# Kernel tuning notes

Measured on AMD Instinct MI355X. Metric: run time of the kernel, lower is better.

The kernel has to match this reference:

```python
import jax, jax.numpy as jnp
import numpy as np

D_MODEL = 1024
N_HEADS = 16
D_HEAD = D_MODEL // N_HEADS
WINDOW = 64
SCALE = 1.0 / np.sqrt(D_HEAD)


def setup_inputs() -> dict:
    key = jax.random.key(0)
    k1, k2, k3 = jax.random.split(key, 3)
    B, N = 1, 4096
    x = jax.random.normal(k1, (B, N, D_MODEL), dtype=jnp.float32)
    # xavier-uniform-ish init for weights (scaled normal is fine for a numeric reference)
    w_qkv = jax.random.normal(k2, (3 * D_MODEL, D_MODEL), dtype=jnp.float32) * (1.0 / np.sqrt(D_MODEL))
    b_qkv = jnp.zeros((3 * D_MODEL,), dtype=jnp.float32)
    w_out = jax.random.normal(k3, (D_MODEL, D_MODEL), dtype=jnp.float32) * (1.0 / np.sqrt(D_MODEL))
    b_out = jnp.zeros((D_MODEL,), dtype=jnp.float32)
    return {"x": x, "w_qkv": w_qkv, "b_qkv": b_qkv, "w_out": w_out, "b_out": b_out}


def reference(x, w_qkv, b_qkv, w_out, b_out):
    B, N, D = x.shape
    # QKV projection (torch Linear: x @ W^T + b)
    qkv = x @ w_qkv.T + b_qkv                      # [B, N, 3D]
    qkv = qkv.reshape(B, N, 3, N_HEADS, D_HEAD)
    qkv = jnp.transpose(qkv, (2, 0, 3, 1, 4))       # [3, B, H, N, dh]
    q, k, v = qkv[0], qkv[1], qkv[2]
    # dense scores, masked to causal sliding window (faithful to original)
    scores = jnp.einsum('bhqd,bhkd->bhqk', q, k) * SCALE  # [B, H, N, N]
    qpos = jnp.arange(N)[:, None]
    kpos = jnp.arange(N)[None, :]
    diff = qpos - kpos
    mask = (diff >= 0) & (diff < WINDOW)            # [N, N]
    scores = jnp.where(mask[None, None, :, :], scores, -jnp.inf)
    attn = jax.nn.softmax(scores, axis=-1)          # every query has >=1 valid key (self)
    out = jnp.einsum('bhqk,bhkd->bhqd', attn, v)    # [B, H, N, dh]
    out = jnp.transpose(out, (0, 2, 1, 3)).reshape(B, N, D)
    out = out @ w_out.T + b_out
    return out
```

## Files before the change

kernel.cpp:

```cpp
#include <hip/hip_runtime.h>
#include <hip/hip_bf16.h>
#include <stdint.h>
#include <stddef.h>

#define NSEQ  4096
#define DM    1024
#define NHEAD 16
#define DHEAD 64
#define WIN   64

using short8 = __attribute__((ext_vector_type(8))) short;
using f32x4  = __attribute__((ext_vector_type(4))) float;

#define GLOBAL_AS __attribute__((address_space(1)))
#define LDS_AS    __attribute__((address_space(3)))

__device__ __forceinline__ unsigned short f2bf(float f) {
  union { float f; unsigned int u; } v; v.f = f;
  unsigned int r = v.u + 0x7FFFu + ((v.u >> 16) & 1u);
  return (unsigned short)(r >> 16);
}

__device__ __forceinline__ void gload_lds16(void* lds, const void* g) {
  __builtin_amdgcn_global_load_lds((const GLOBAL_AS unsigned int*)g,
                                   (LDS_AS unsigned int*)lds, 16, 0, 0);
}

#define NX4 1048576
#define NW4 786432
__global__ void cvt_all(const float* __restrict__ x,
                        const float* __restrict__ wqkv,
                        const float* __restrict__ wout,
                        unsigned short* __restrict__ dst) {
  int i = blockIdx.x * blockDim.x + threadIdx.x;
  float4 f;
  if (i < NX4)            f = ((const float4*)x)[i];
  else if (i < NX4 + NW4) f = ((const float4*)wqkv)[i - NX4];
  else                    f = ((const float4*)wout)[i - (NX4 + NW4)];
  ushort4 o;
  o.x = f2bf(f.x); o.y = f2bf(f.y); o.z = f2bf(f.z); o.w = f2bf(f.w);
  ((ushort4*)dst)[i] = o;
}

__global__ __launch_bounds__(512, 1)
void gemm_qkv(const unsigned short* __restrict__ A,
              const unsigned short* __restrict__ B,
              const float* __restrict__ bias,
              unsigned short* __restrict__ qo,
              unsigned short* __restrict__ ko,
              unsigned short* __restrict__ vo) {
  __shared__ short lds[57344];

  const int bm = blockIdx.x >> 4;
  const int bn = blockIdx.x & 15;
  const int m0 = bm << 8, n0 = bn * 192;
  const int tid = threadIdx.x, w = tid >> 6, l = tid & 63;
  const int wr = w >> 2, wc = w & 3;
  const int l15 = l & 15, l4 = l >> 4;
  const int srow = l >> 2;
  const int skel = ((l & 3) << 3) ^ ((l >= 32) << 4);
  const int roff = l15 * 32 + ((l4 * 8) ^ ((l15 >= 8) * 16));

  f32x4 acc[8][3] = {};

  auto stageA = [&](int j, int qm) {
    const int base = (j & 1) * 28672 + qm * 8192;
#pragma unroll
    for (int r = 0; r < 2; ++r) {
      const int c = r * 8 + w;
      gload_lds16(&lds[base + c * 512 + l * 8],
                  A + (size_t)(m0 + qm * 128 + (c >> 1) * 16 + srow) * 1024
                    + (j << 6) + (c & 1) * 32 + skel);
    }
  };
  auto stageB = [&](int j, int qk) {
    const int base = (j & 1) * 28672 + 16384 + qk * 6144;
    {
      const int c = w;
      gload_lds16(&lds[base + c * 512 + l * 8],
                  B + (size_t)(n0 + c * 16 + srow) * 1024
                    + (j << 6) + qk * 32 + skel);
    }
    {
      const int c = 8 + (w & 3);
      gload_lds16(&lds[base + c * 512 + l * 8],
                  B + (size_t)(n0 + c * 16 + srow) * 1024
                    + (j << 6) + qk * 32 + skel);
    }
  };

  stageA(0, 0); stageA(0, 1); stageB(0, 1); stageB(0, 0); stageB(1, 0);
  asm volatile("s_waitcnt vmcnt(2)" ::: "memory");
  __builtin_amdgcn_s_barrier();

  const int NT = 16;
  for (int j = 0; j < NT; ++j) {
    const int buf = (j & 1) * 28672;
    const short* Ah = &lds[buf + wr * 8192];
#pragma unroll
    for (int p = 0; p < 4; ++p) {
      const int qm = p & 1, qk = p >> 1;
      const short* Bh = &lds[buf + 16384 + qk * 6144];
      short8 af[4], bf[3];
#pragma unroll
      for (int i = 0; i < 4; ++i)
        af[i] = *(const short8*)&Ah[(qm * 4 + i) * 1024 + qk * 512 + roff];
#pragma unroll
      for (int ni = 0; ni < 3; ++ni)
        bf[ni] = *(const short8*)&Bh[(wc * 3 + ni) * 512 + roff];
      if (p == 0 && j + 1 < NT) { stageA(j + 1, 0); stageA(j + 1, 1); stageB(j + 1, 1); }
      if (p == 2 && j + 2 < NT) { stageB(j + 2, 0); }
      if (p == 3) {
        if (j + 2 < NT) asm volatile("s_waitcnt vmcnt(2)" ::: "memory");
        else            asm volatile("s_waitcnt vmcnt(0)" ::: "memory");
      } else {
        asm volatile("" ::: "memory");
      }
      __builtin_amdgcn_s_barrier();
      __builtin_amdgcn_s_setprio(1);
#pragma unroll
      for (int i = 0; i < 4; ++i)
#pragma unroll
        for (int ni = 0; ni < 3; ++ni)
          acc[qm * 4 + i][ni] = __builtin_amdgcn_mfma_f32_16x16x32_bf16(
              af[i], bf[ni], acc[qm * 4 + i][ni], 0, 0, 0);
      __builtin_amdgcn_s_setprio(0);
    }
  }

#pragma unroll
  for (int ni = 0; ni < 3; ++ni) {
    const int n  = n0 + wc * 48 + ni * 16 + l15;
    const float bv = bias[n];
    const int region = n >> 10;
#pragma unroll
    for (int mi = 0; mi < 8; ++mi) {
      const int mb = m0 + wr * 128 + mi * 16 + l4 * 4;
      if (region == 0) {
        const int h = (n >> 6) & 15, d = n & 63;
#pragma unroll
        for (int r = 0; r < 4; ++r)
          qo[((size_t)(h * NSEQ + mb + r)) * DHEAD + d] =
              f2bf((acc[mi][ni][r] + bv) * 0.125f);
      } else if (region == 1) {
        const int nn = n - 1024;
        const int h = nn >> 6, d = nn & 63;
#pragma unroll
        for (int r = 0; r < 4; ++r)
          ko[((size_t)(h * NSEQ + mb + r)) * DHEAD + d] =
              f2bf(acc[mi][ni][r] + bv);
      } else {
        const int nn = n - 2048;
        ushort4 pk;
        pk.x = f2bf(acc[mi][ni][0] + bv);
        pk.y = f2bf(acc[mi][ni][1] + bv);
        pk.z = f2bf(acc[mi][ni][2] + bv);
        pk.w = f2bf(acc[mi][ni][3] + bv);
        *(ushort4*)&vo[(size_t)nn * NSEQ + mb] = pk;
      }
    }
  }
}

__global__ __launch_bounds__(256)
void gemm_op(const unsigned short* __restrict__ A,
             const unsigned short* __restrict__ B,
             const float* __restrict__ bias,
             float* __restrict__ Cf) {
  __shared__ short lds[3][8192];

  const int bm = blockIdx.x >> 4;
  const int bn = blockIdx.x & 15;
  const int m0 = bm << 6, n0 = bn << 6;
  const int tid = threadIdx.x, w = tid >> 6, l = tid & 63;
  const int wr = w >> 1, wc = w & 1;
  const int l15 = l & 15, l4 = l >> 4;
  const int srow = l >> 2;
  const int skel = ((l & 3) << 3) ^ ((l >= 32) << 4);
  const int roff = l15 * 32 + ((l4 * 8) ^ ((l15 >= 8) * 16));

  f32x4 acc[2][2] = {};
  const int NT = 16;

  auto stage = [&](int t) {
    const int buf = t % 3;
    const int kb  = t << 6;
#pragma unroll
    for (int r = 0; r < 2; ++r) {
      const int c = r * 4 + w;
      gload_lds16(&lds[buf][c * 512 + l * 8],
                  A + (size_t)(m0 + (c >> 1) * 16 + srow) * 1024
                    + kb + (c & 1) * 32 + skel);
      gload_lds16(&lds[buf][4096 + c * 512 + l * 8],
                  B + (size_t)(n0 + (c >> 1) * 16 + srow) * 1024
                    + kb + (c & 1) * 32 + skel);
    }
  };

  stage(0);
  stage(1);
  asm volatile("s_waitcnt vmcnt(4)" ::: "memory");
  __builtin_amdgcn_s_barrier();

  for (int t = 0; t < NT; ++t) {
    const short* Ab = &lds[t % 3][0];
    const short* Bb = &lds[t % 3][4096];
    short8 af[2][2], bf[2][2];
#pragma unroll
    for (int mi = 0; mi < 2; ++mi)
#pragma unroll
      for (int kk = 0; kk < 2; ++kk)
        af[mi][kk] = *(const short8*)&Ab[((wr * 2 + mi) * 2 + kk) * 512 + roff];
#pragma unroll
    for (int ni = 0; ni < 2; ++ni)
#pragma unroll
      for (int kk = 0; kk < 2; ++kk)
        bf[ni][kk] = *(const short8*)&Bb[((wc * 2 + ni) * 2 + kk) * 512 + roff];
    if (t + 2 < NT) {
      stage(t + 2);
      asm volatile("s_waitcnt vmcnt(4)" ::: "memory");
    } else if (t + 2 == NT) {
      asm volatile("s_waitcnt vmcnt(0)" ::: "memory");
    }
    __builtin_amdgcn_s_barrier();
    __builtin_amdgcn_s_setprio(1);
#pragma unroll
    for (int kk = 0; kk < 2; ++kk)
#pragma unroll
      for (int mi = 0; mi < 2; ++mi)
#pragma unroll
        for (int ni = 0; ni < 2; ++ni)
          acc[mi][ni] = __builtin_amdgcn_mfma_f32_16x16x32_bf16(
              af[mi][kk], bf[ni][kk], acc[mi][ni], 0, 0, 0);
    __builtin_amdgcn_s_setprio(0);
  }

#pragma unroll
  for (int ni = 0; ni < 2; ++ni) {
    const int n  = n0 + wc * 32 + ni * 16 + l15;
    const float bv = bias[n];
#pragma unroll
    for (int mi = 0; mi < 2; ++mi) {
      const int mb = m0 + wr * 32 + mi * 16 + l4 * 4;
#pragma unroll
      for (int r = 0; r < 4; ++r)
        Cf[(size_t)(mb + r) * DM + n] = acc[mi][ni][r] + bv;
    }
  }
}

__global__ __launch_bounds__(256)
void attn_kernel(const unsigned short* __restrict__ Qb,
                 const unsigned short* __restrict__ Kb,
                 const unsigned short* __restrict__ Vt,
                 unsigned short* __restrict__ att) {
  __shared__ short Pl[4][16][136];
  const int h  = blockIdx.x >> 6;
  const int q0 = (blockIdx.x & 63) << 6;
  const int w  = threadIdx.x >> 6;
  const int l  = threadIdx.x & 63;
  const int l15 = l & 15, l4 = l >> 4;
  const int qw = q0 + w * 16;

  const unsigned short* Qh = Qb + (size_t)h * NSEQ * DHEAD;
  const unsigned short* Kh = Kb + (size_t)h * NSEQ * DHEAD;
  const unsigned short* Vh = Vt + (size_t)h * DHEAD * NSEQ;

  short8 aq[2];
  {
    const int qrow = qw + l15;
    aq[0] = *(const short8*)&Qh[(size_t)qrow * DHEAD + l4 * 8];
    aq[1] = *(const short8*)&Qh[(size_t)qrow * DHEAD + 32 + l4 * 8];
  }

  f32x4 s[8] = {};
#pragma unroll
  for (int t = 0; t < 8; ++t) {
    int j  = q0 - 64 + t * 16 + l15;
    int jc = j < 0 ? 0 : j;
    short8 b0 = *(const short8*)&Kh[(size_t)jc * DHEAD + l4 * 8];
    short8 b1 = *(const short8*)&Kh[(size_t)jc * DHEAD + 32 + l4 * 8];
    s[t] = __builtin_amdgcn_mfma_f32_16x16x32_bf16(aq[0], b0, s[t], 0, 0, 0);
    s[t] = __builtin_amdgcn_mfma_f32_16x16x32_bf16(aq[1], b1, s[t], 0, 0, 0);
  }

  float rmax[4] = {-3e38f, -3e38f, -3e38f, -3e38f};
#pragma unroll
  for (int t = 0; t < 8; ++t)
#pragma unroll
    for (int r = 0; r < 4; ++r) {
      const int i = qw + l4 * 4 + r;
      const int j = q0 - 64 + t * 16 + l15;
      const int diff = i - j;
      float sv = (j >= 0 && diff >= 0 && diff < WIN) ? s[t][r] : -3e38f;
      s[t][r] = sv;
      rmax[r] = fmaxf(rmax[r], sv);
    }
#pragma unroll
  for (int r = 0; r < 4; ++r)
#pragma unroll
    for (int m = 1; m < 16; m <<= 1)
      rmax[r] = fmaxf(rmax[r], __shfl_xor(rmax[r], m, 64));

  float rsum[4] = {0.f, 0.f, 0.f, 0.f};
#pragma unroll
  for (int t = 0; t < 8; ++t)
#pragma unroll
    for (int r = 0; r < 4; ++r) {
      float p = __expf(s[t][r] - rmax[r]);
      s[t][r] = p;
      rsum[r] += p;
    }
#pragma unroll
  for (int r = 0; r < 4; ++r)
#pragma unroll
    for (int m = 1; m < 16; m <<= 1)
      rsum[r] += __shfl_xor(rsum[r], m, 64);

#pragma unroll
  for (int t = 0; t < 8; ++t)
#pragma unroll
    for (int r = 0; r < 4; ++r)
      Pl[w][l4 * 4 + r][t * 16 + l15] = (short)f2bf(s[t][r]);

  f32x4 o[4] = {};
#pragma unroll
  for (int ks = 0; ks < 4; ++ks) {
    short8 ap = *(const short8*)&Pl[w][l15][ks * 32 + l4 * 8];
    int jg = q0 - 64 + ks * 32 + l4 * 8;
    if (jg < 0) jg = 0;
#pragma unroll
    for (int dt = 0; dt < 4; ++dt) {
      const int d = dt * 16 + l15;
      short8 bv = *(const short8*)&Vh[(size_t)d * NSEQ + jg];
      o[dt] = __builtin_amdgcn_mfma_f32_16x16x32_bf16(ap, bv, o[dt], 0, 0, 0);
    }
  }

#pragma unroll
  for (int r = 0; r < 4; ++r) {
    const float rinv = 1.0f / rsum[r];
    const int m = qw + l4 * 4 + r;
#pragma unroll
    for (int dt = 0; dt < 4; ++dt)
      att[(size_t)m * DM + h * DHEAD + dt * 16 + l15] = f2bf(o[dt][r] * rinv);
  }
}

extern "C" void kernel_launch(void* const* d_in, const int* in_sizes, int n_in,
                              void* d_out, int out_size, void* d_ws, size_t ws_size,
                              hipStream_t stream) {
  const float* x    = (const float*)d_in[0];
  const float* wqkv = (const float*)d_in[1];
  const float* bqkv = (const float*)d_in[2];
  const float* wout = (const float*)d_in[3];
  const float* bout = (const float*)d_in[4];
  float* out = (float*)d_out;

  unsigned short* ws = (unsigned short*)d_ws;
  unsigned short* xb    = ws;
  unsigned short* wqkvb = xb    + (size_t)NSEQ * DM;
  unsigned short* woutb = wqkvb + (size_t)3 * DM * DM;
  unsigned short* qb    = woutb + (size_t)DM * DM;
  unsigned short* kb    = qb    + (size_t)NSEQ * DM;
  unsigned short* vtb   = kb    + (size_t)NSEQ * DM;
  unsigned short* attb  = vtb   + (size_t)NSEQ * DM;

  cvt_all<<<8192, 256, 0, stream>>>(x, wqkv, wout, xb);

  gemm_qkv<<<16 * 16, 512, 0, stream>>>(xb, wqkvb, bqkv, qb, kb, vtb);

  attn_kernel<<<NHEAD * (NSEQ / 64), 256, 0, stream>>>(qb, kb, vtb, attb);

  gemm_op<<<64 * 16, 256, 0, stream>>>(attb, woutb, bout, out);
}
```

Measured before the change: 85.71 us.

## Skip fully masked key tiles in attention and use double-buffered GEMM pipeline

The attention kernel now computes only 6 of the 8 key tiles per wave, and only 3 of the 4 PV k-steps. It chooses the tiles from the wave index so that keys entirely outside that wave's causal window are skipped. This cuts MFMA work and K/V loads in the attention stage. Separately, the output-projection GEMM changes from a triple-buffered LDS pipeline with explicit vmcnt waits to a double-buffered one that synchronises with __syncthreads each iteration. That lowers LDS use but may expose more load latency.

```diff
diff --git a/kernel.cpp b/kernel.cpp
--- a/kernel.cpp
+++ b/kernel.cpp
@@ -167,7 +167,7 @@
              const unsigned short* __restrict__ B,
              const float* __restrict__ bias,
              float* __restrict__ Cf) {
-  __shared__ short lds[3][8192];
+  __shared__ short lds[2][8192];
 
   const int bm = blockIdx.x >> 4;
   const int bn = blockIdx.x & 15;
@@ -183,7 +183,7 @@
   const int NT = 16;
 
   auto stage = [&](int t) {
-    const int buf = t % 3;
+    const int buf = t & 1;
     const int kb  = t << 6;
 #pragma unroll
     for (int r = 0; r < 2; ++r) {
@@ -198,13 +198,11 @@
   };
 
   stage(0);
-  stage(1);
-  asm volatile("s_waitcnt vmcnt(4)" ::: "memory");
-  __builtin_amdgcn_s_barrier();
-
   for (int t = 0; t < NT; ++t) {
-    const short* Ab = &lds[t % 3][0];
-    const short* Bb = &lds[t % 3][4096];
+    __syncthreads();
+    if (t + 1 < NT) stage(t + 1);
+    const short* Ab = &lds[t & 1][0];
+    const short* Bb = &lds[t & 1][4096];
     short8 af[2][2], bf[2][2];
 #pragma unroll
     for (int mi = 0; mi < 2; ++mi)
@@ -216,13 +214,6 @@
 #pragma unroll
       for (int kk = 0; kk < 2; ++kk)
         bf[ni][kk] = *(const short8*)&Bb[((wc * 2 + ni) * 2 + kk) * 512 + roff];
-    if (t + 2 < NT) {
-      stage(t + 2);
-      asm volatile("s_waitcnt vmcnt(4)" ::: "memory");
-    } else if (t + 2 == NT) {
-      asm volatile("s_waitcnt vmcnt(0)" ::: "memory");
-    }
-    __builtin_amdgcn_s_barrier();
     __builtin_amdgcn_s_setprio(1);
 #pragma unroll
     for (int kk = 0; kk < 2; ++kk)
@@ -261,6 +252,7 @@
   const int l  = threadIdx.x & 63;
   const int l15 = l & 15, l4 = l >> 4;
   const int qw = q0 + w * 16;
+  const int tb = w & ~1;
 
   const unsigned short* Qh = Qb + (size_t)h * NSEQ * DHEAD;
   const unsigned short* Kh = Kb + (size_t)h * NSEQ * DHEAD;
@@ -273,27 +265,27 @@
     aq[1] = *(const short8*)&Qh[(size_t)qrow * DHEAD + 32 + l4 * 8];
   }
 
-  f32x4 s[8] = {};
-#pragma unroll
-  for (int t = 0; t < 8; ++t) {
-    int j  = q0 - 64 + t * 16 + l15;
+  f32x4 s[6] = {};
+#pragma unroll
+  for (int tt = 0; tt < 6; ++tt) {
+    int j  = q0 - 64 + (tb + tt) * 16 + l15;
     int jc = j < 0 ? 0 : j;
     short8 b0 = *(const short8*)&Kh[(size_t)jc * DHEAD + l4 * 8];
     short8 b1 = *(const short8*)&Kh[(size_t)jc * DHEAD + 32 + l4 * 8];
-    s[t] = __builtin_amdgcn_mfma_f32_16x16x32_bf16(aq[0], b0, s[t], 0, 0, 0);
-    s[t] = __builtin_amdgcn_mfma_f32_16x16x32_bf16(aq[1], b1, s[t], 0, 0, 0);
+    s[tt] = __builtin_amdgcn_mfma_f32_16x16x32_bf16(aq[0], b0, s[tt], 0, 0, 0);
+    s[tt] = __builtin_amdgcn_mfma_f32_16x16x32_bf16(aq[1], b1, s[tt], 0, 0, 0);
   }
 
   float rmax[4] = {-3e38f, -3e38f, -3e38f, -3e38f};
 #pragma unroll
-  for (int t = 0; t < 8; ++t)
+  for (int tt = 0; tt < 6; ++tt)
 #pragma unroll
     for (int r = 0; r < 4; ++r) {
       const int i = qw + l4 * 4 + r;
-      const int j = q0 - 64 + t * 16 + l15;
+      const int j = q0 - 64 + (tb + tt) * 16 + l15;
       const int diff = i - j;
-      float sv = (j >= 0 && diff >= 0 && diff < WIN) ? s[t][r] : -3e38f;
-      s[t][r] = sv;
+      float sv = (j >= 0 && diff >= 0 && diff < WIN) ? s[tt][r] : -3e38f;
+      s[tt][r] = sv;
       rmax[r] = fmaxf(rmax[r], sv);
     }
 #pragma unroll
@@ -304,11 +296,11 @@
 
   float rsum[4] = {0.f, 0.f, 0.f, 0.f};
 #pragma unroll
-  for (int t = 0; t < 8; ++t)
+  for (int tt = 0; tt < 6; ++tt)
 #pragma unroll
     for (int r = 0; r < 4; ++r) {
-      float p = __expf(s[t][r] - rmax[r]);
-      s[t][r] = p;
+      float p = __expf(s[tt][r] - rmax[r]);
+      s[tt][r] = p;
       rsum[r] += p;
     }
 #pragma unroll
@@ -318,14 +310,15 @@
       rsum[r] += __shfl_xor(rsum[r], m, 64);
 
 #pragma unroll
-  for (int t = 0; t < 8; ++t)
+  for (int tt = 0; tt < 6; ++tt)
 #pragma unroll
     for (int r = 0; r < 4; ++r)
-      Pl[w][l4 * 4 + r][t * 16 + l15] = (short)f2bf(s[t][r]);
+      Pl[w][l4 * 4 + r][(tb + tt) * 16 + l15] = (short)f2bf(s[tt][r]);
 
   f32x4 o[4] = {};
 #pragma unroll
-  for (int ks = 0; ks < 4; ++ks) {
+  for (int kq = 0; kq < 3; ++kq) {
+    const int ks = (w >> 1) + kq;
     short8 ap = *(const short8*)&Pl[w][l15][ks * 32 + l4 * 8];
     int jg = q0 - 64 + ks * 32 + l4 * 8;
     if (jg < 0) jg = 0;
```

Result: faster. 82.19 us (-4.1%).
